# Performance work log

Measured on AMD Instinct MI355X. Metric: run time of the kernel, lower is better.

Reference implementation:

```python
import jax, jax.numpy as jnp
import numpy as np

GAMMA = 0.05
EPS = 1e-12
H, NH, HD = 768, 12, 64

def _lin(x, W, b):
    return x @ W.T + b

def _pproc(x, W, b):
    # LRP gamma-rule projection: forward value equals _lin(x, W, b); gradient flows through the gamma-modified layer times a detached ratio.
    z = _lin(x, W, b)
    zp = _lin(x, W + GAMMA * jnp.clip(W, 0.0, None), b + GAMMA * jnp.clip(b, 0.0, None))
    return zp * jax.lax.stop_gradient(z / zp)

def setup_inputs() -> dict:
    key = jax.random.key(0)
    ks = jax.random.split(key, 9)
    s = 0.02
    d = {"hidden_states": jax.random.normal(ks[0], (2, 2048, H), jnp.float32)}
    for i, n in enumerate(["q", "k", "v", "o"]):
        d["W" + n] = jax.random.normal(ks[1 + 2 * i], (H, H), jnp.float32) * s
        d["b" + n] = jax.random.normal(ks[2 + 2 * i], (H,), jnp.float32) * s
    return d

def reference(hidden_states, Wq, bq, Wk, bk, Wv, bv, Wo, bo):
    B, S, _ = hidden_states.shape
    def heads(x):  # [B,S,H] -> [B,NH,S,HD]
        return x.reshape(B, S, NH, HD).transpose(0, 2, 1, 3)
    q = heads(_pproc(hidden_states, Wq, bq))
    k = heads(_pproc(hidden_states, Wk, bk))
    v = heads(_pproc(hidden_states, Wv, bv))
    # NOTE: source has NO 1/sqrt(d_head) scaling on the scores
    scores = jnp.einsum("bhsd,bhtd->bhst", q, k)
    probs = jax.lax.stop_gradient(jax.nn.softmax(scores, axis=-1))  # detach_kq branch
    ctx = jnp.einsum("bhst,bhtd->bhsd", probs, v).transpose(0, 2, 1, 3).reshape(B, S, H)
    # BertSelfOutput.pforward: gamma-modified dense applied directly (no pproc ratio)
    pWo = Wo + GAMMA * jnp.clip(Wo, 0.0, None)
    pbo = bo + GAMMA * jnp.clip(bo, 0.0, None)
    y = _lin(ctx, pWo, pbo) + hidden_states
    # 'nowb' LayerNorm with detached mean and std (torch.std -> unbiased, ddof=1)
    mean = jax.lax.stop_gradient(jnp.mean(y, axis=-1, keepdims=True))
    std = jax.lax.stop_gradient(jnp.std(y, axis=-1, keepdims=True, ddof=1))
    out = (y - mean) / (std + EPS)
    return out, probs
```

## Files before the change

### kernel.cpp

```cpp
#include <hip/hip_runtime.h>

#define GAMMA 0.05f
#define LNEPS 1e-12f
#define HDIMT 768
#define SDIM  2048
#define NHEAD 12
#define HDHEAD 64
#define MTOT  4096
#define BHEADS 24
#define OUT0E ((size_t)MTOT * HDIMT)
#define NXEL  ((size_t)MTOT * HDIMT)
#define WNEL  ((size_t)HDIMT * HDIMT)
#define NEATT ((size_t)BHEADS * SDIM * HDHEAD)

typedef __attribute__((ext_vector_type(8))) short short8;
typedef __attribute__((ext_vector_type(4))) float f32x4;
typedef __attribute__((ext_vector_type(16))) float f32x16;

#define MFMA16(a, b, c) __builtin_amdgcn_mfma_f32_16x16x32_bf16((a), (b), (c), 0, 0, 0)
#define MFMA32(a, b, c) __builtin_amdgcn_mfma_f32_32x32x16_bf16((a), (b), (c), 0, 0, 0)

__device__ __forceinline__ float bf2f(unsigned short u) {
    union { unsigned int i; float f; } c; c.i = ((unsigned int)u) << 16; return c.f;
}
__device__ __forceinline__ unsigned short f2bf(float f) {
    union { float f; unsigned int i; } c; c.f = f;
    unsigned int i = c.i;
    i += 0x7FFFu + ((i >> 16) & 1u);
    return (unsigned short)(i >> 16);
}
__device__ __forceinline__ void splitbf(float v, unsigned short& h, unsigned short& l) {
    h = f2bf(v);
    l = f2bf(v - bf2f(h));
}

__device__ __forceinline__ void load8f(const void* p, size_t idx, int isbf, float* r) {
    if (isbf) {
        const unsigned short* b = (const unsigned short*)p + idx;
        uint4 u = *(const uint4*)b;
        const unsigned short* pu = (const unsigned short*)&u;
        #pragma unroll
        for (int j = 0; j < 8; ++j) r[j] = bf2f(pu[j]);
    } else {
        const float* f = (const float*)p + idx;
        float4 a = *(const float4*)f, c = *(const float4*)(f + 4);
        r[0] = a.x; r[1] = a.y; r[2] = a.z; r[3] = a.w;
        r[4] = c.x; r[5] = c.y; r[6] = c.z; r[7] = c.w;
    }
}
__device__ __forceinline__ float load1f(const void* p, size_t idx, int isbf) {
    return isbf ? bf2f(((const unsigned short*)p)[idx]) : ((const float*)p)[idx];
}

__global__ void detect_kernel(const void* __restrict__ x, int* __restrict__ flag) {
    __shared__ int cnt;
    if (threadIdx.x == 0) cnt = 0;
    __syncthreads();
    const unsigned short* u = (const unsigned short*)x;
    unsigned short v = u[2 * threadIdx.x];
    int e = (v >> 7) & 0xFF;
    int ok = (e >= 100 && e <= 140) ? 1 : 0;
    atomicAdd(&cnt, ok);
    __syncthreads();
    if (threadIdx.x == 0) flag[0] = (cnt >= 192) ? 1 : 0;
}

__global__ __launch_bounds__(256) void prep_kernel(
    const void* __restrict__ x,
    const void* __restrict__ Wq, const void* __restrict__ Wk,
    const void* __restrict__ Wv, const void* __restrict__ Wo,
    unsigned short* __restrict__ xh, unsigned short* __restrict__ xl,
    unsigned short* __restrict__ wqh, unsigned short* __restrict__ wql,
    unsigned short* __restrict__ wkh, unsigned short* __restrict__ wkl,
    unsigned short* __restrict__ wvh, unsigned short* __restrict__ wvl,
    unsigned short* __restrict__ woh, unsigned short* __restrict__ wol,
    const int* __restrict__ flag)
{
    const int isbf = flag[0];
    const int z = blockIdx.y;
    const size_t i8 = ((size_t)blockIdx.x * 256 + threadIdx.x) * 8;
    const void* src; unsigned short* dh; unsigned short* dl;
    size_t n; int gam = 0;
    if (z == 0)      { src = x;  dh = xh;  dl = xl;  n = NXEL; }
    else if (z == 1) { src = Wq; dh = wqh; dl = wql; n = WNEL; }
    else if (z == 2) { src = Wk; dh = wkh; dl = wkl; n = WNEL; }
    else if (z == 3) { src = Wv; dh = wvh; dl = wvl; n = WNEL; }
    else             { src = Wo; dh = woh; dl = wol; n = WNEL; gam = 1; }
    if (i8 >= n) return;

    float v[8]; load8f(src, i8, isbf, v);
    alignas(16) unsigned short hv[8], lv[8];
    #pragma unroll
    for (int j = 0; j < 8; ++j) {
        float f = v[j];
        if (gam) f += GAMMA * fmaxf(f, 0.0f);
        splitbf(f, hv[j], lv[j]);
    }
    *(uint4*)(dh + i8) = *(const uint4*)hv;
    *(uint4*)(dl + i8) = *(const uint4*)lv;
}

#define FRAG(buf, row, kb)                                                        \
    (*(const short8*)((const char*)(buf) +                                        \
                      (((row) << 7) + ((kb) ^ (((row) & 7) << 4)))))

__global__ __launch_bounds__(256) void qkv_mfma(
    const unsigned short* __restrict__ xh, const unsigned short* __restrict__ xl,
    const unsigned short* __restrict__ wqh, const unsigned short* __restrict__ wql,
    const unsigned short* __restrict__ wkh, const unsigned short* __restrict__ wkl,
    const unsigned short* __restrict__ wvh, const unsigned short* __restrict__ wvl,
    const void* __restrict__ bq, const void* __restrict__ bk, const void* __restrict__ bv,
    unsigned short* __restrict__ qh, unsigned short* __restrict__ ql,
    unsigned short* __restrict__ kh, unsigned short* __restrict__ kl,
    unsigned short* __restrict__ vth, unsigned short* __restrict__ vtl,
    const int* __restrict__ flag)
{
    __shared__ alignas(16) unsigned short Ah[8192], Al[8192];
    __shared__ alignas(16) unsigned short Bh[4096], Bl[4096];

    const int isbf = flag[0];
    const int tid = threadIdx.x;
    const int lane = tid & 63, w = tid >> 6;
    const int l15 = lane & 15, g = lane >> 4;
    const int m0 = blockIdx.x * 128;
    const int h  = blockIdx.y;
    const int z  = blockIdx.z;

    const unsigned short* Wh = (z == 0) ? wqh : (z == 1) ? wkh : wvh;
    const unsigned short* Wl = (z == 0) ? wql : (z == 1) ? wkl : wvl;
    const void* bias = (z == 0) ? bq : (z == 1) ? bk : bv;

    f32x4 acc[2][4];
    #pragma unroll
    for (int i = 0; i < 2; ++i)
        #pragma unroll
        for (int c = 0; c < 4; ++c) acc[i][c] = (f32x4){0.0f, 0.0f, 0.0f, 0.0f};

    for (int k0 = 0; k0 < HDIMT; k0 += 64) {
        __syncthreads();
        #pragma unroll
        for (int p = 0; p < 4; ++p) {
            const int idx = tid + p * 256;
            const int row = idx >> 3, slot = idx & 7;
            const int off = (row << 7) + ((slot << 4) ^ ((row & 7) << 4));
            const size_t s = (size_t)(m0 + row) * HDIMT + k0 + slot * 8;
            *(uint4*)((char*)Ah + off) = *(const uint4*)(xh + s);
            *(uint4*)((char*)Al + off) = *(const uint4*)(xl + s);
        }
        #pragma unroll
        for (int p = 0; p < 2; ++p) {
            const int idx = tid + p * 256;
            const int row = idx >> 3, slot = idx & 7;
            const int off = (row << 7) + ((slot << 4) ^ ((row & 7) << 4));
            const size_t s = (size_t)(h * 64 + row) * HDIMT + k0 + slot * 8;
            *(uint4*)((char*)Bh + off) = *(const uint4*)(Wh + s);
            *(uint4*)((char*)Bl + off) = *(const uint4*)(Wl + s);
        }
        __syncthreads();

        #pragma unroll
        for (int ks = 0; ks < 2; ++ks) {
            const int kb = (g << 4) + (ks << 6);
            short8 a8h[2], a8l[2], b8h[4], b8l[4];
            #pragma unroll
            for (int i = 0; i < 2; ++i) {
                const int row = w * 32 + i * 16 + l15;
                a8h[i] = FRAG(Ah, row, kb);
                a8l[i] = FRAG(Al, row, kb);
            }
            #pragma unroll
            for (int c = 0; c < 4; ++c) {
                const int row = c * 16 + l15;
                b8h[c] = FRAG(Bh, row, kb);
                b8l[c] = FRAG(Bl, row, kb);
            }
            #pragma unroll
            for (int i = 0; i < 2; ++i)
                #pragma unroll
                for (int c = 0; c < 4; ++c) {
                    acc[i][c] = MFMA16(a8h[i], b8h[c], acc[i][c]);
                    acc[i][c] = MFMA16(a8l[i], b8h[c], acc[i][c]);
                    acc[i][c] = MFMA16(a8h[i], b8l[c], acc[i][c]);
                }
        }
    }

    float bb[4];
    #pragma unroll
    for (int c = 0; c < 4; ++c) bb[c] = load1f(bias, h * 64 + c * 16 + l15, isbf);

    if (z < 2) {
        unsigned short* oh = z ? kh : qh;
        unsigned short* ol = z ? kl : ql;
        #pragma unroll
        for (int i = 0; i < 2; ++i)
            #pragma unroll
            for (int c = 0; c < 4; ++c)
                #pragma unroll
                for (int r = 0; r < 4; ++r) {
                    const int m = m0 + w * 32 + i * 16 + g * 4 + r;
                    const int b = m >> 11, s = m & 2047;
                    const int d = c * 16 + l15;
                    unsigned short hu, lu;
                    splitbf(acc[i][c][r] + bb[c], hu, lu);
                    const size_t o = ((size_t)(b * NHEAD + h) * SDIM + s) * HDHEAD + d;
                    oh[o] = hu; ol[o] = lu;
                }
    } else {
        #pragma unroll
        for (int i = 0; i < 2; ++i)
            #pragma unroll
            for (int c = 0; c < 4; ++c) {
                const int m00 = m0 + w * 32 + i * 16 + g * 4;
                const int b = m00 >> 11, s0 = m00 & 2047;
                const int d = c * 16 + l15;
                ushort4 hv, lv;
                unsigned short* hp = (unsigned short*)&hv;
                unsigned short* lp = (unsigned short*)&lv;
                #pragma unroll
                for (int r = 0; r < 4; ++r)
                    splitbf(acc[i][c][r] + bb[c], hp[r], lp[r]);
                const size_t o = ((size_t)(b * NHEAD + h) * HDHEAD + d) * SDIM + s0;
                *(ushort4*)(vth + o) = hv;
                *(ushort4*)(vtl + o) = lv;
            }
    }
}

#define STAGE64(dsth, dstl, srch, srcl, SROW)                                     \
    {                                                                             \
        _Pragma("unroll")                                                         \
        for (int p_ = 0; p_ < 2; ++p_) {                                          \
            const int idx_ = tid + p_ * 256;                                      \
            const int row_ = idx_ >> 3, slot_ = idx_ & 7;                         \
            const int off_ = (row_ << 7) + ((slot_ << 4) ^ ((row_ & 7) << 4));    \
            *(uint4*)((char*)(dsth) + off_) =                                     \
                *(const uint4*)((srch) + (size_t)row_ * (SROW) + slot_ * 8);      \
            *(uint4*)((char*)(dstl) + off_) =                                     \
                *(const uint4*)((srcl) + (size_t)row_ * (SROW) + slot_ * 8);      \
        }                                                                         \
    }

__global__ __launch_bounds__(256) void attn_kernel(
    const unsigned short* __restrict__ qh, const unsigned short* __restrict__ ql,
    const unsigned short* __restrict__ kh, const unsigned short* __restrict__ kl,
    const unsigned short* __restrict__ vth, const unsigned short* __restrict__ vtl,
    unsigned short* __restrict__ ctxh, unsigned short* __restrict__ ctxl,
    void* __restrict__ dout,
    const int* __restrict__ flag)
{
    __shared__ alignas(16) unsigned short Qh[4096], Ql[4096];
    __shared__ alignas(16) unsigned short Kh[4096], Kl[4096];
    __shared__ alignas(16) unsigned short Vh[4096], Vl[4096];
    __shared__ float lsums[64][2];
    __shared__ float linv[64];

    const int isbf = flag[0];
    const int tid  = threadIdx.x;
    const int lane = tid & 63;
    const int w    = tid >> 6;
    const int l31  = lane & 31, g2 = lane >> 5;
    const int qh_  = (w >> 1) * 32;
    const int th_  = (w & 1) * 32;
    const int bh   = blockIdx.y;
    const int r0   = blockIdx.x * 64;

    {
        const unsigned short* sh = qh + ((size_t)bh * SDIM + r0) * HDHEAD;
        const unsigned short* sl = ql + ((size_t)bh * SDIM + r0) * HDHEAD;
        STAGE64(Qh, Ql, sh, sl, HDHEAD);
    }
    __syncthreads();

    short8 aqh[4], aql[4];
    #pragma unroll
    for (int ks = 0; ks < 4; ++ks) {
        const int kb = ks * 32 + g2 * 16;
        aqh[ks] = FRAG(Qh, qh_ + l31, kb);
        aql[ks] = FRAG(Ql, qh_ + l31, kb);
    }

    float lsum[16];
    #pragma unroll
    for (int r = 0; r < 16; ++r) lsum[r] = 0.0f;

    for (int kt = 0; kt < 32; ++kt) {
        __syncthreads();
        {
            const unsigned short* sh = kh + ((size_t)bh * SDIM + kt * 64) * HDHEAD;
            const unsigned short* sl = kl + ((size_t)bh * SDIM + kt * 64) * HDHEAD;
            STAGE64(Kh, Kl, sh, sl, HDHEAD);
        }
        __syncthreads();

        f32x16 acc = {};
        #pragma unroll
        for (int ks = 0; ks < 4; ++ks) {
            const int kb = ks * 32 + g2 * 16;
            short8 b8h = FRAG(Kh, th_ + l31, kb);
            short8 b8l = FRAG(Kl, th_ + l31, kb);
            acc = MFMA32(aqh[ks], b8h, acc);
            acc = MFMA32(aql[ks], b8h, acc);
            acc = MFMA32(aqh[ks], b8l, acc);
        }
        #pragma unroll
        for (int r = 0; r < 16; ++r) lsum[r] += __expf(acc[r]);
    }

    #pragma unroll
    for (int d = 1; d < 32; d <<= 1) {
        #pragma unroll
        for (int r = 0; r < 16; ++r) lsum[r] += __shfl_xor(lsum[r], d, 64);
    }
    if (l31 == 0) {
        #pragma unroll
        for (int r = 0; r < 16; ++r) {
            const int qrow = qh_ + (r & 3) + 8 * (r >> 2) + 4 * g2;
            lsums[qrow][w & 1] = lsum[r];
        }
    }
    __syncthreads();
    if (tid < 64) linv[tid] = 1.0f / (lsums[tid][0] + lsums[tid][1]);
    __syncthreads();

    float invr[16];
    #pragma unroll
    for (int r = 0; r < 16; ++r)
        invr[r] = linv[qh_ + (r & 3) + 8 * (r >> 2) + 4 * g2];

    f32x16 cacc = {};

    for (int kt = 0; kt < 32; ++kt) {
        __syncthreads();
        {
            const unsigned short* sh = kh + ((size_t)bh * SDIM + kt * 64) * HDHEAD;
            const unsigned short* sl = kl + ((size_t)bh * SDIM + kt * 64) * HDHEAD;
            STAGE64(Kh, Kl, sh, sl, HDHEAD);
            const unsigned short* vh = vth + (size_t)bh * HDHEAD * SDIM + (size_t)(kt * 64);
            const unsigned short* vl = vtl + (size_t)bh * HDHEAD * SDIM + (size_t)(kt * 64);
            STAGE64(Vh, Vl, vh, vl, SDIM);
        }
        __syncthreads();

        f32x16 acc = {};
        #pragma unroll
        for (int ks = 0; ks < 4; ++ks) {
            const int kb = ks * 32 + g2 * 16;
            short8 b8h = FRAG(Kh, th_ + l31, kb);
            short8 b8l = FRAG(Kl, th_ + l31, kb);
            acc = MFMA32(aqh[ks], b8h, acc);
            acc = MFMA32(aql[ks], b8h, acc);
            acc = MFMA32(aqh[ks], b8l, acc);
        }
        __syncthreads();

        #pragma unroll
        for (int r = 0; r < 16; ++r) {
            const float p = __expf(acc[r]) * invr[r];
            const int q = qh_ + (r & 3) + 8 * (r >> 2) + 4 * g2;
            const int t = th_ + l31;
            unsigned short ph_, pl_;
            splitbf(p, ph_, pl_);
            const int off = (q << 7) + ((t << 1) ^ ((q & 7) << 4));
            *(unsigned short*)((char*)Kh + off) = ph_;
            *(unsigned short*)((char*)Kl + off) = pl_;
        }
        __syncthreads();

        {
            const int prow = tid >> 2, pt0 = (tid & 3) * 16;
            const int swz = (prow & 7) << 4;
            const int o0 = (prow << 7) + (((pt0 << 1) + 0) ^ swz);
            const int o1 = (prow << 7) + (((pt0 << 1) + 16) ^ swz);
            const size_t go = OUT0E + ((size_t)bh * SDIM + (r0 + prow)) * SDIM
                            + (size_t)(kt * 64 + pt0);
            uint4 h0 = *(const uint4*)((const char*)Kh + o0);
            uint4 h1 = *(const uint4*)((const char*)Kh + o1);
            if (isbf) {
                *(uint4*)((unsigned short*)dout + go)     = h0;
                *(uint4*)((unsigned short*)dout + go + 8) = h1;
            } else {
                uint4 l0 = *(const uint4*)((const char*)Kl + o0);
                uint4 l1 = *(const uint4*)((const char*)Kl + o1);
                const unsigned short* hp0 = (const unsigned short*)&h0;
                const unsigned short* lp0 = (const unsigned short*)&l0;
                const unsigned short* hp1 = (const unsigned short*)&h1;
                const unsigned short* lp1 = (const unsigned short*)&l1;
                float* op = (float*)dout + go;
                #pragma unroll
                for (int j = 0; j < 8; ++j) op[j]     = bf2f(hp0[j]) + bf2f(lp0[j]);
                #pragma unroll
                for (int j = 0; j < 8; ++j) op[8 + j] = bf2f(hp1[j]) + bf2f(lp1[j]);
            }
        }

        #pragma unroll
        for (int ks = 0; ks < 4; ++ks) {
            const int kb = ks * 32 + g2 * 16;
            short8 pah = FRAG(Kh, qh_ + l31, kb);
            short8 pal = FRAG(Kl, qh_ + l31, kb);
            short8 v8h = FRAG(Vh, th_ + l31, kb);
            short8 v8l = FRAG(Vl, th_ + l31, kb);
            cacc = MFMA32(pah, v8h, cacc);
            cacc = MFMA32(pal, v8h, cacc);
            cacc = MFMA32(pah, v8l, cacc);
        }
    }

    const int bb_ = bh / NHEAD, hh_ = bh % NHEAD;
    #pragma unroll
    for (int r = 0; r < 16; ++r) {
        const int q = qh_ + (r & 3) + 8 * (r >> 2) + 4 * g2;
        const int d = th_ + l31;
        unsigned short hu, lu;
        splitbf(cacc[r], hu, lu);
        const size_t o = ((size_t)(bb_ * SDIM + r0 + q)) * HDIMT + hh_ * HDHEAD + d;
        ctxh[o] = hu; ctxl[o] = lu;
    }
}

__global__ __launch_bounds__(256) void oproj_mfma(
    const unsigned short* __restrict__ ctxh, const unsigned short* __restrict__ ctxl,
    const unsigned short* __restrict__ woh, const unsigned short* __restrict__ wol,
    const void* __restrict__ bo, const void* __restrict__ x,
    float* __restrict__ y, const int* __restrict__ flag)
{
    __shared__ alignas(16) unsigned short Ah[8192], Al[8192];
    __shared__ alignas(16) unsigned short Bh[4096], Bl[4096];

    const int isbf = flag[0];
    const int tid = threadIdx.x;
    const int lane = tid & 63, w = tid >> 6;
    const int l15 = lane & 15, g = lane >> 4;
    const int m0 = blockIdx.x * 128;
    const int h  = blockIdx.y;

    f32x4 acc[2][4];
    #pragma unroll
    for (int i = 0; i < 2; ++i)
        #pragma unroll
        for (int c = 0; c < 4; ++c) acc[i][c] = (f32x4){0.0f, 0.0f, 0.0f, 0.0f};

    for (int k0 = 0; k0 < HDIMT; k0 += 64) {
        __syncthreads();
        #pragma unroll
        for (int p = 0; p < 4; ++p) {
            const int idx = tid + p * 256;
            const int row = idx >> 3, slot = idx & 7;
            const int off = (row << 7) + ((slot << 4) ^ ((row & 7) << 4));
            const size_t s = (size_t)(m0 + row) * HDIMT + k0 + slot * 8;
            *(uint4*)((char*)Ah + off) = *(const uint4*)(ctxh + s);
            *(uint4*)((char*)Al + off) = *(const uint4*)(ctxl + s);
        }
        #pragma unroll
        for (int p = 0; p < 2; ++p) {
            const int idx = tid + p * 256;
            const int row = idx >> 3, slot = idx & 7;
            const int off = (row << 7) + ((slot << 4) ^ ((row & 7) << 4));
            const size_t s = (size_t)(h * 64 + row) * HDIMT + k0 + slot * 8;
            *(uint4*)((char*)Bh + off) = *(const uint4*)(woh + s);
            *(uint4*)((char*)Bl + off) = *(const uint4*)(wol + s);
        }
        __syncthreads();

        #pragma unroll
        for (int ks = 0; ks < 2; ++ks) {
            const int kb = (g << 4) + (ks << 6);
            short8 a8h[2], a8l[2], b8h[4], b8l[4];
            #pragma unroll
            for (int i = 0; i < 2; ++i) {
                const int row = w * 32 + i * 16 + l15;
                a8h[i] = FRAG(Ah, row, kb);
                a8l[i] = FRAG(Al, row, kb);
            }
            #pragma unroll
            for (int c = 0; c < 4; ++c) {
                const int row = c * 16 + l15;
                b8h[c] = FRAG(Bh, row, kb);
                b8l[c] = FRAG(Bl, row, kb);
            }
            #pragma unroll
            for (int i = 0; i < 2; ++i)
                #pragma unroll
                for (int c = 0; c < 4; ++c) {
                    acc[i][c] = MFMA16(a8h[i], b8h[c], acc[i][c]);
                    acc[i][c] = MFMA16(a8l[i], b8h[c], acc[i][c]);
                    acc[i][c] = MFMA16(a8h[i], b8l[c], acc[i][c]);
                }
        }
    }

    float pb[4];
    #pragma unroll
    for (int c = 0; c < 4; ++c) {
        float t = load1f(bo, h * 64 + c * 16 + l15, isbf);
        pb[c] = t + GAMMA * fmaxf(t, 0.0f);
    }

    #pragma unroll
    for (int i = 0; i < 2; ++i)
        #pragma unroll
        for (int c = 0; c < 4; ++c)
            #pragma unroll
            for (int r = 0; r < 4; ++r) {
                const int m = m0 + w * 32 + i * 16 + g * 4 + r;
                const int n = h * 64 + c * 16 + l15;
                const size_t o = (size_t)m * HDIMT + n;
                y[o] = acc[i][c][r] + pb[c] + load1f(x, o, isbf);
            }
}

__global__ __launch_bounds__(256) void ln_kernel(
    const float* __restrict__ y, void* __restrict__ out,
    const int* __restrict__ flag)
{
    __shared__ float part[8];
    const int isbf = flag[0];
    const int m = blockIdx.x;
    const int tid = threadIdx.x;
    const int lane = tid & 63, w = tid >> 6;
    const float* yr = y + (size_t)m * HDIMT;

    float v0 = yr[tid], v1 = yr[tid + 256], v2 = yr[tid + 512];

    float s = v0 + v1 + v2;
    #pragma unroll
    for (int d = 1; d < 64; d <<= 1) s += __shfl_xor(s, d, 64);
    if (lane == 0) part[w] = s;
    __syncthreads();
    const float mean = (part[0] + part[1] + part[2] + part[3]) * (1.0f / 768.0f);

    const float d0 = v0 - mean, d1 = v1 - mean, d2 = v2 - mean;
    float ss = d0 * d0 + d1 * d1 + d2 * d2;
    #pragma unroll
    for (int d = 1; d < 64; d <<= 1) ss += __shfl_xor(ss, d, 64);
    if (lane == 0) part[4 + w] = ss;
    __syncthreads();
    const float var = (part[4] + part[5] + part[6] + part[7]) * (1.0f / 767.0f);
    const float inv = 1.0f / (sqrtf(var) + LNEPS);

    const size_t base = (size_t)m * HDIMT;
    if (isbf) {
        unsigned short* o = (unsigned short*)out;
        o[base + tid]       = f2bf(d0 * inv);
        o[base + tid + 256] = f2bf(d1 * inv);
        o[base + tid + 512] = f2bf(d2 * inv);
    } else {
        float* o = (float*)out;
        o[base + tid]       = d0 * inv;
        o[base + tid + 256] = d1 * inv;
        o[base + tid + 512] = d2 * inv;
    }
}

extern "C" void kernel_launch(void* const* d_in, const int* in_sizes, int n_in,
                              void* d_out, int out_size, void* d_ws, size_t ws_size,
                              hipStream_t stream)
{
    (void)in_sizes; (void)n_in; (void)out_size; (void)ws_size;

    const void* x  = d_in[0];
    const void* Wq = d_in[1];
    const void* bq = d_in[2];
    const void* Wk = d_in[3];
    const void* bk = d_in[4];
    const void* Wv = d_in[5];
    const void* bv = d_in[6];
    const void* Wo = d_in[7];
    const void* bo = d_in[8];

    unsigned short* qh  = (unsigned short*)d_ws;
    unsigned short* ql  = qh  + NEATT;
    unsigned short* kh  = ql  + NEATT;
    unsigned short* kl  = kh  + NEATT;
    unsigned short* vth = kl  + NEATT;
    unsigned short* vtl = vth + NEATT;
    unsigned short* xh  = vtl + NEATT;
    unsigned short* xl  = xh  + NXEL;
    unsigned short* wqh = xl  + NXEL;
    unsigned short* wql = wqh + WNEL;
    unsigned short* wkh = wql + WNEL;
    unsigned short* wkl = wkh + WNEL;
    unsigned short* wvh = wkl + WNEL;
    unsigned short* wvl = wvh + WNEL;
    unsigned short* woh = wvl + WNEL;
    unsigned short* wol = woh + WNEL;
    int* flag = (int*)(wol + WNEL);

    float* y = (float*)qh;
    unsigned short* ctxh = xh;
    unsigned short* ctxl = xl;

    detect_kernel<<<1, 256, 0, stream>>>(x, flag);
    prep_kernel<<<dim3(1536, 5), 256, 0, stream>>>(x, Wq, Wk, Wv, Wo,
                                                   xh, xl, wqh, wql, wkh, wkl,
                                                   wvh, wvl, woh, wol, flag);
    qkv_mfma<<<dim3(32, 12, 3), 256, 0, stream>>>(xh, xl, wqh, wql, wkh, wkl, wvh, wvl,
                                                  bq, bk, bv,
                                                  qh, ql, kh, kl, vth, vtl, flag);
    attn_kernel<<<dim3(32, 24), 256, 0, stream>>>(qh, ql, kh, kl, vth, vtl,
                                                  ctxh, ctxl, d_out, flag);
    oproj_mfma<<<dim3(32, 12), 256, 0, stream>>>(ctxh, ctxl, woh, wol, bo, x, y, flag);
    ln_kernel<<<MTOT, 256, 0, stream>>>(y, d_out, flag);
}
```

Measured before the change: 748.2 us.

## Reduce split-bf16 precision in attention and double-buffer K in sum pass

V is now stored as a single bf16 value rather than a hi/lo pair, and P·V runs as one MFMA instead of three. In the first (row-sum) pass, QK^T drops the K-lo term and uses a double-buffered K tile in LDS, so one barrier per tile is removed. Probabilities are written straight from registers to global memory with scalar stores, replacing the LDS round-trip and vectorized copy. This cuts MFMA work, LDS traffic and V memory, but lowers the accuracy of the row sums and the context, and the scattered global stores of probs may coalesce poorly.

```diff
diff --git a/kernel.cpp b/kernel.cpp
--- a/kernel.cpp
+++ b/kernel.cpp
@@ -112,7 +112,7 @@
     const void* __restrict__ bq, const void* __restrict__ bk, const void* __restrict__ bv,
     unsigned short* __restrict__ qh, unsigned short* __restrict__ ql,
     unsigned short* __restrict__ kh, unsigned short* __restrict__ kl,
-    unsigned short* __restrict__ vth, unsigned short* __restrict__ vtl,
+    unsigned short* __restrict__ vth,
     const int* __restrict__ flag)
 {
     __shared__ alignas(16) unsigned short Ah[8192], Al[8192];
@@ -214,15 +214,12 @@
                 const int m00 = m0 + w * 32 + i * 16 + g * 4;
                 const int b = m00 >> 11, s0 = m00 & 2047;
                 const int d = c * 16 + l15;
-                ushort4 hv, lv;
+                ushort4 hv;
                 unsigned short* hp = (unsigned short*)&hv;
-                unsigned short* lp = (unsigned short*)&lv;
                 #pragma unroll
-                for (int r = 0; r < 4; ++r)
-                    splitbf(acc[i][c][r] + bb[c], hp[r], lp[r]);
+                for (int r = 0; r < 4; ++r) hp[r] = f2bf(acc[i][c][r] + bb[c]);
                 const size_t o = ((size_t)(b * NHEAD + h) * HDHEAD + d) * SDIM + s0;
                 *(ushort4*)(vth + o) = hv;
-                *(ushort4*)(vtl + o) = lv;
             }
     }
 }
@@ -241,17 +238,30 @@
         }                                                                         \
     }
 
+#define STAGE64H(dst, src, SROW)                                                  \
+    {                                                                             \
+        _Pragma("unroll")                                                         \
+        for (int p_ = 0; p_ < 2; ++p_) {                                          \
+            const int idx_ = tid + p_ * 256;                                      \
+            const int row_ = idx_ >> 3, slot_ = idx_ & 7;                         \
+            const int off_ = (row_ << 7) + ((slot_ << 4) ^ ((row_ & 7) << 4));    \
+            *(uint4*)((char*)(dst) + off_) =                                      \
+                *(const uint4*)((src) + (size_t)row_ * (SROW) + slot_ * 8);       \
+        }                                                                         \
+    }
+
 __global__ __launch_bounds__(256) void attn_kernel(
     const unsigned short* __restrict__ qh, const unsigned short* __restrict__ ql,
     const unsigned short* __restrict__ kh, const unsigned short* __restrict__ kl,
-    const unsigned short* __restrict__ vth, const unsigned short* __restrict__ vtl,
+    const unsigned short* __restrict__ vth,
     unsigned short* __restrict__ ctxh, unsigned short* __restrict__ ctxl,
     void* __restrict__ dout,
     const int* __restrict__ flag)
 {
     __shared__ alignas(16) unsigned short Qh[4096], Ql[4096];
     __shared__ alignas(16) unsigned short Kh[4096], Kl[4096];
-    __shared__ alignas(16) unsigned short Vh[4096], Vl[4096];
+    __shared__ alignas(16) unsigned short Vh[4096];
+    __shared__ alignas(16) unsigned short Ph[4096];
     __shared__ float lsums[64][2];
     __shared__ float linv[64];
 
@@ -265,6 +275,10 @@
     const int bh   = blockIdx.y;
     const int r0   = blockIdx.x * 64;
 
+    const unsigned short* kbh = kh + (size_t)bh * SDIM * HDHEAD;
+    const unsigned short* kbl = kl + (size_t)bh * SDIM * HDHEAD;
+    const unsigned short* vb  = vth + (size_t)bh * HDHEAD * SDIM;
+
     {
         const unsigned short* sh = qh + ((size_t)bh * SDIM + r0) * HDHEAD;
         const unsigned short* sl = ql + ((size_t)bh * SDIM + r0) * HDHEAD;
@@ -284,13 +298,54 @@
     #pragma unroll
     for (int r = 0; r < 16; ++r) lsum[r] = 0.0f;
 
+    STAGE64H(Kh, kbh, HDHEAD);
     for (int kt = 0; kt < 32; ++kt) {
         __syncthreads();
-        {
-            const unsigned short* sh = kh + ((size_t)bh * SDIM + kt * 64) * HDHEAD;
-            const unsigned short* sl = kl + ((size_t)bh * SDIM + kt * 64) * HDHEAD;
-            STAGE64(Kh, Kl, sh, sl, HDHEAD);
-        }
+        unsigned short* cur = (kt & 1) ? Kl : Kh;
+        unsigned short* nxt = (kt & 1) ? Kh : Kl;
+        if (kt < 31) STAGE64H(nxt, kbh + (size_t)(kt + 1) * 64 * HDHEAD, HDHEAD);
+
+        f32x16 acc = {};
+        #pragma unroll
+        for (int ks = 0; ks < 4; ++ks) {
+            const int kb = ks * 32 + g2 * 16;
+            short8 b8 = FRAG(cur, th_ + l31, kb);
+            acc = MFMA32(aqh[ks], b8, acc);
+            acc = MFMA32(aql[ks], b8, acc);
+        }
+        #pragma unroll
+        for (int r = 0; r < 16; ++r) lsum[r] += __expf(acc[r]);
+    }
+
+    #pragma unroll
+    for (int d = 1; d < 32; d <<= 1) {
+        #pragma unroll
+        for (int r = 0; r < 16; ++r) lsum[r] += __shfl_xor(lsum[r], d, 64);
+    }
+    if (l31 == 0) {
+        #pragma unroll
+        for (int r = 0; r < 16; ++r) {
+            const int qrow = qh_ + (r & 3) + 8 * (r >> 2) + 4 * g2;
+            lsums[qrow][w & 1] = lsum[r];
+        }
+    }
+    __syncthreads();
+    if (tid < 64) linv[tid] = 1.0f / (lsums[tid][0] + lsums[tid][1]);
+    __syncthreads();
+
+    float invr[16];
+    #pragma unroll
+    for (int r = 0; r < 16; ++r)
+        invr[r] = linv[qh_ + (r & 3) + 8 * (r >> 2) + 4 * g2];
+
+    f32x16 cacc = {};
+    const size_t grow = OUT0E + ((size_t)bh * SDIM + r0) * SDIM;
+
+    for (int kt = 0; kt < 32; ++kt) {
+        __syncthreads();
+        STAGE64(Kh, Kl, kbh + (size_t)kt * 64 * HDHEAD,
+                        kbl + (size_t)kt * 64 * HDHEAD, HDHEAD);
+        STAGE64H(Vh, vb + (size_t)(kt * 64), SDIM);
         __syncthreads();
 
         f32x16 acc = {};
@@ -303,107 +358,26 @@
             acc = MFMA32(aql[ks], b8h, acc);
             acc = MFMA32(aqh[ks], b8l, acc);
         }
-        #pragma unroll
-        for (int r = 0; r < 16; ++r) lsum[r] += __expf(acc[r]);
-    }
-
-    #pragma unroll
-    for (int d = 1; d < 32; d <<= 1) {
-        #pragma unroll
-        for (int r = 0; r < 16; ++r) lsum[r] += __shfl_xor(lsum[r], d, 64);
-    }
-    if (l31 == 0) {
-        #pragma unroll
-        for (int r = 0; r < 16; ++r) {
-            const int qrow = qh_ + (r & 3) + 8 * (r >> 2) + 4 * g2;
-            lsums[qrow][w & 1] = lsum[r];
-        }
-    }
-    __syncthreads();
-    if (tid < 64) linv[tid] = 1.0f / (lsums[tid][0] + lsums[tid][1]);
-    __syncthreads();
-
-    float invr[16];
-    #pragma unroll
-    for (int r = 0; r < 16; ++r)
-        invr[r] = linv[qh_ + (r & 3) + 8 * (r >> 2) + 4 * g2];
-
-    f32x16 cacc = {};
-
-    for (int kt = 0; kt < 32; ++kt) {
-        __syncthreads();
-        {
-            const unsigned short* sh = kh + ((size_t)bh * SDIM + kt * 64) * HDHEAD;
-            const unsigned short* sl = kl + ((size_t)bh * SDIM + kt * 64) * HDHEAD;
-            STAGE64(Kh, Kl, sh, sl, HDHEAD);
-            const unsigned short* vh = vth + (size_t)bh * HDHEAD * SDIM + (size_t)(kt * 64);
-            const unsigned short* vl = vtl + (size_t)bh * HDHEAD * SDIM + (size_t)(kt * 64);
-            STAGE64(Vh, Vl, vh, vl, SDIM);
-        }
-        __syncthreads();
-
-        f32x16 acc = {};
-        #pragma unroll
-        for (int ks = 0; ks < 4; ++ks) {
-            const int kb = ks * 32 + g2 * 16;
-            short8 b8h = FRAG(Kh, th_ + l31, kb);
-            short8 b8l = FRAG(Kl, th_ + l31, kb);
-            acc = MFMA32(aqh[ks], b8h, acc);
-            acc = MFMA32(aql[ks], b8h, acc);
-            acc = MFMA32(aqh[ks], b8l, acc);
-        }
-        __syncthreads();
-
+
+        const int tcol = th_ + l31;
+        const int gcol = kt * 64 + tcol;
         #pragma unroll
         for (int r = 0; r < 16; ++r) {
             const float p = __expf(acc[r]) * invr[r];
             const int q = qh_ + (r & 3) + 8 * (r >> 2) + 4 * g2;
-            const int t = th_ + l31;
-            unsigned short ph_, pl_;
-            splitbf(p, ph_, pl_);
-            const int off = (q << 7) + ((t << 1) ^ ((q & 7) << 4));
-            *(unsigned short*)((char*)Kh + off) = ph_;
-            *(unsigned short*)((char*)Kl + off) = pl_;
-        }
-        __syncthreads();
-
-        {
-            const int prow = tid >> 2, pt0 = (tid & 3) * 16;
-            const int swz = (prow & 7) << 4;
-            const int o0 = (prow << 7) + (((pt0 << 1) + 0) ^ swz);
-            const int o1 = (prow << 7) + (((pt0 << 1) + 16) ^ swz);
-            const size_t go = OUT0E + ((size_t)bh * SDIM + (r0 + prow)) * SDIM
-                            + (size_t)(kt * 64 + pt0);
-            uint4 h0 = *(const uint4*)((const char*)Kh + o0);
-            uint4 h1 = *(const uint4*)((const char*)Kh + o1);
-            if (isbf) {
-                *(uint4*)((unsigned short*)dout + go)     = h0;
-                *(uint4*)((unsigned short*)dout + go + 8) = h1;
-            } else {
-                uint4 l0 = *(const uint4*)((const char*)Kl + o0);
-                uint4 l1 = *(const uint4*)((const char*)Kl + o1);
-                const unsigned short* hp0 = (const unsigned short*)&h0;
-                const unsigned short* lp0 = (const unsigned short*)&l0;
-                const unsigned short* hp1 = (const unsigned short*)&h1;
-                const unsigned short* lp1 = (const unsigned short*)&l1;
-                float* op = (float*)dout + go;
-                #pragma unroll
-                for (int j = 0; j < 8; ++j) op[j]     = bf2f(hp0[j]) + bf2f(lp0[j]);
-                #pragma unroll
-                for (int j = 0; j < 8; ++j) op[8 + j] = bf2f(hp1[j]) + bf2f(lp1[j]);
-            }
-        }
+            if (isbf) ((unsigned short*)dout)[grow + (size_t)q * SDIM + gcol] = f2bf(p);
+            else      ((float*)dout)[grow + (size_t)q * SDIM + gcol] = p;
+            const int off = (q << 7) + ((tcol << 1) ^ ((q & 7) << 4));
+            *(unsigned short*)((char*)Ph + off) = f2bf(p);
+        }
+        __syncthreads();
 
         #pragma unroll
         for (int ks = 0; ks < 4; ++ks) {
             const int kb = ks * 32 + g2 * 16;
-            short8 pah = FRAG(Kh, qh_ + l31, kb);
-            short8 pal = FRAG(Kl, qh_ + l31, kb);
-            short8 v8h = FRAG(Vh, th_ + l31, kb);
-            short8 v8l = FRAG(Vl, th_ + l31, kb);
-            cacc = MFMA32(pah, v8h, cacc);
-            cacc = MFMA32(pal, v8h, cacc);
-            cacc = MFMA32(pah, v8l, cacc);
+            short8 pa = FRAG(Ph, qh_ + l31, kb);
+            short8 v8 = FRAG(Vh, th_ + l31, kb);
+            cacc = MFMA32(pa, v8, cacc);
         }
     }
 
@@ -574,8 +548,7 @@
     unsigned short* kh  = ql  + NEATT;
     unsigned short* kl  = kh  + NEATT;
     unsigned short* vth = kl  + NEATT;
-    unsigned short* vtl = vth + NEATT;
-    unsigned short* xh  = vtl + NEATT;
+    unsigned short* xh  = vth + NEATT;
     unsigned short* xl  = xh  + NXEL;
     unsigned short* wqh = xl  + NXEL;
     unsigned short* wql = wqh + WNEL;
@@ -597,8 +570,8 @@
                                                    wvh, wvl, woh, wol, flag);
     qkv_mfma<<<dim3(32, 12, 3), 256, 0, stream>>>(xh, xl, wqh, wql, wkh, wkl, wvh, wvl,
                                                   bq, bk, bv,
-                                                  qh, ql, kh, kl, vth, vtl, flag);
-    attn_kernel<<<dim3(32, 24), 256, 0, stream>>>(qh, ql, kh, kl, vth, vtl,
+                                                  qh, ql, kh, kl, vth, flag);
+    attn_kernel<<<dim3(32, 24), 256, 0, stream>>>(qh, ql, kh, kl, vth,
                                                   ctxh, ctxl, d_out, flag);
     oproj_mfma<<<dim3(32, 12), 256, 0, stream>>>(ctxh, ctxl, woh, wol, bo, x, y, flag);
     ln_kernel<<<MTOT, 256, 0, stream>>>(y, d_out, flag);
```

After: 772.2 us. 3.2% more time.
